# Kernel optimization log

Hardware: AMD Instinct MI355X
Metric: run time of the kernel (lower is better)

The kernel has to match this reference:

```python
import jax, jax.numpy as jnp
import numpy as np

B, LP, LQ, D, H = 4, 256, 256, 256, 256


def setup_inputs() -> dict:
    key = jax.random.key(0)
    ks = jax.random.split(key, 10)
    s_d = 1.0 / np.sqrt(D)
    s_h = 1.0 / np.sqrt(H)
    return {
        "Hp": jax.random.normal(ks[0], (B, LP, D), jnp.float32),
        "Hq": jax.random.normal(ks[1], (B, LQ, D), jnp.float32),
        # weights stored as (in, out); torch Linear does x @ W.T
        "Wc1": jax.random.normal(ks[2], (D, H), jnp.float32) * s_d,
        "Wc2": jax.random.normal(ks[3], (D, H), jnp.float32) * s_d,
        "vc": jax.random.normal(ks[4], (H,), jnp.float32) * s_h,
        "Wb": jax.random.normal(ks[5], (D, D), jnp.float32) * s_d,
        "Wd": jax.random.normal(ks[6], (D, H), jnp.float32) * s_d,
        "vd": jax.random.normal(ks[7], (H,), jnp.float32) * s_h,
        "Wm": jax.random.normal(ks[8], (D, H), jnp.float32) * s_d,
        "vm": jax.random.normal(ks[9], (H,), jnp.float32) * s_h,
    }


def _attend(scores, Hq):
    # scores: (B, Lp, Lq); softmax over Lq then weighted sum of Hq
    a = jax.nn.softmax(scores, axis=2)
    return jnp.einsum("bpq,bqd->bpd", a, Hq)


def reference(Hp, Hq, Wc1, Wc2, vc, Wb, Wd, vd, Wm, vm):
    # branch c: additive attention. tanh(Wc1 Hq + Wc2 Hp) . vc
    s1 = Hq @ Wc1                      # (B, Lq, H)
    s2 = Hp @ Wc2                      # (B, Lp, H)
    sc = jnp.einsum("bpqh,h->bpq", jnp.tanh(s1[:, None, :, :] + s2[:, :, None, :]), vc)
    qc = _attend(sc, Hq)

    # branch b: bilinear attention Hp (Wb Hq)^T
    sb = jnp.einsum("bpd,bqd->bpq", Hp, Hq @ Wb)
    qb = _attend(sb, Hq)

    # branch d: multiplicative interaction. tanh(Wd (Hq * Hp)) . vd
    sd = jnp.einsum("bpqh,h->bpq",
                    jnp.tanh(jnp.einsum("bqk,bpk,kh->bpqh", Hq, Hp, Wd)), vd)
    qd = _attend(sd, Hq)

    # branch m: subtractive interaction. tanh(Wm (Hq - Hp)) . vm
    m1 = Hq @ Wm                       # (B, Lq, H)
    m2 = Hp @ Wm                       # (B, Lp, H)
    sm = jnp.einsum("bpqh,h->bpq", jnp.tanh(m1[:, None, :, :] - m2[:, :, None, :]), vm)
    qm = _attend(sm, Hq)

    return (qc, qb, qd, qm)
```

## Files before the change

### kernel.cpp

```cpp
#include <hip/hip_runtime.h>

#define LOG2E 1.4426950408889634f
#define TANH_S 2.8853900817779268f
#define NB 4
#define NL 256
#define ND 256
#define NH 256

typedef __attribute__((ext_vector_type(8))) short s16x8;
typedef __attribute__((ext_vector_type(4))) short s16x4;
typedef __attribute__((ext_vector_type(4))) float f32x4;
typedef __attribute__((ext_vector_type(2))) unsigned int u32x2;
typedef __attribute__((ext_vector_type(4))) unsigned int u32x4;

static __device__ __forceinline__ float b2f(unsigned short u) {
  return __builtin_bit_cast(float, (unsigned int)u << 16);
}
static __device__ __forceinline__ unsigned short f2b(float f) {
  unsigned int x = __builtin_bit_cast(unsigned int, f);
  return (unsigned short)((x + 0x7fffu + ((x >> 16) & 1u)) >> 16);
}
static __device__ __forceinline__ unsigned int cvtpk(float lo, float hi) {
  unsigned int r;
  asm("v_cvt_pk_bf16_f32 %0, %1, %2" : "=v"(r) : "v"(lo), "v"(hi));
  return r;
}


__global__ void __launch_bounds__(256) prep(
    const float* __restrict__ Hq,
    const float* __restrict__ Wc1, const float* __restrict__ Wc2,
    const float* __restrict__ Wb, const float* __restrict__ Wm,
    const float* __restrict__ Wd, float* __restrict__ ws)
{
  const int which = blockIdx.y;
  const int tid = threadIdx.x;
  __shared__ __align__(16) float a_s[8][256];
  if (which == 0) {
    const int m0 = blockIdx.x * 8;
    unsigned short* AF = (unsigned short*)((char*)ws + 3145728);
    const int row = m0 + (tid >> 5);
    const int grp = tid & 31;
    const int kt = grp >> 2, quad = grp & 3;
    const int k0 = kt * 32 + quad * 8;
    const int bb = row >> 8, q = row & 255;
    const int w = q >> 6, mt = (q >> 4) & 3, c16 = q & 15;
    const float* src = Hq + row * ND + k0;
    f32x4 v0 = *(const f32x4*)(src);
    f32x4 v1 = *(const f32x4*)(src + 4);
    s16x8 o;
    #pragma unroll
    for (int j = 0; j < 4; ++j) { o[j] = (short)f2b(v0[j]); o[4 + j] = (short)f2b(v1[j]); }
    *(s16x8*)(AF + ((((bb * 4 + w) * 4 + mt) * 8 + kt) * 64 + quad * 16 + c16) * 8) = o;
    return;
  }
  if (which == 1) {
    if (blockIdx.x >= 32) return;
    const int k0 = blockIdx.x * 8;
    #pragma unroll
    for (int kk = 0; kk < 8; ++kk)
      a_s[kk][tid] = Wd[(k0 + kk) * NH + tid] * TANH_S;
    __syncthreads();
    float* WdT = (float*)((char*)ws + 4718592);
    f32x4 v0 = {a_s[0][tid], a_s[1][tid], a_s[2][tid], a_s[3][tid]};
    f32x4 v1 = {a_s[4][tid], a_s[5][tid], a_s[6][tid], a_s[7][tid]};
    *(f32x4*)(WdT + tid * 256 + k0) = v0;
    *(f32x4*)(WdT + tid * 256 + k0 + 4) = v1;
    return;
  }
  const int w = blockIdx.x >> 5;
  const int k0 = (blockIdx.x & 31) * 8;
  const float* W = (w == 0) ? Wc1 : (w == 1) ? Wm : (w == 2) ? Wb : Wc2;
  const float scale = (w == 2) ? 1.0f : TANH_S;
  #pragma unroll
  for (int kk = 0; kk < 8; ++kk)
    a_s[kk][tid] = W[(k0 + kk) * NH + tid] * scale;
  __syncthreads();
  unsigned short* WT = (unsigned short*)((char*)ws + 3670016) + w * 131072;
  s16x8 hi, lo;
  #pragma unroll
  for (int kk = 0; kk < 8; ++kk) {
    float v = a_s[kk][tid];
    unsigned short h = f2b(v);
    hi[kk] = (short)h;
    lo[kk] = (short)f2b(v - b2f(h));
  }
  *(s16x8*)(WT + tid * 256 + k0) = hi;
  *(s16x8*)(WT + 65536 + tid * 256 + k0) = lo;
}

__global__ void __launch_bounds__(256) gemm5(
    const float* __restrict__ Hq, const float* __restrict__ Hp,
    float* __restrict__ ws)
{
  const int rt = blockIdx.x, ct = blockIdx.y, mz = blockIdx.z;
  const int tid = threadIdx.x;
  const int wave = tid >> 6, lane = tid & 63;
  const int quad = lane >> 4, c16 = lane & 15;

  __shared__ __align__(16) char bs[32768];
  char* BsH = bs;
  char* BsL = bs + 16384;

  const int w = (mz == 4) ? 1 : ((mz == 3) ? 3 : mz);
  const float* A = (mz >= 3) ? Hp : Hq;
  const int n0 = ct * 32;

  {
    const unsigned short* WTw = (const unsigned short*)((const char*)ws + 3670016)
                                + w * 131072 + n0 * 256;
    const int soff = (tid & 31) * 16;
    #pragma unroll
    for (int i = 0; i < 4; ++i) {
      const int h = i * 8 + (tid >> 5);
      const int doff = h * 512 + (soff ^ ((h & 7) * 16));
      u32x4 vh = *(const u32x4*)((const char*)WTw + h * 512 + soff);
      u32x4 vl = *(const u32x4*)((const char*)WTw + 131072 + h * 512 + soff);
      *(u32x4*)(BsH + doff) = vh;
      *(u32x4*)(BsL + doff) = vl;
    }
  }

  const int row = rt * 64 + wave * 16 + c16;
  s16x8 ah[8], al[8];
  #pragma unroll
  for (int kt = 0; kt < 8; ++kt) {
    const float* src = A + row * ND + kt * 32 + quad * 8;
    f32x4 v0 = *(const f32x4*)(src);
    f32x4 v1 = *(const f32x4*)(src + 4);
    #pragma unroll
    for (int j = 0; j < 4; ++j) {
      unsigned short h0 = f2b(v0[j]);
      ah[kt][j] = (short)h0;
      al[kt][j] = (short)f2b(v0[j] - b2f(h0));
      unsigned short h1 = f2b(v1[j]);
      ah[kt][4 + j] = (short)h1;
      al[kt][4 + j] = (short)f2b(v1[j] - b2f(h1));
    }
  }
  __syncthreads();

  f32x4 acc[2];
  #pragma unroll
  for (int nt = 0; nt < 2; ++nt) acc[nt] = f32x4{0.f, 0.f, 0.f, 0.f};

  const int xswz = (c16 & 7) * 16;
  #pragma unroll
  for (int kt = 0; kt < 8; ++kt) {
    #pragma unroll
    for (int nt = 0; nt < 2; ++nt) {
      const int baddr = (nt * 16 + c16) * 512 + ((kt * 64 + quad * 16) ^ xswz);
      s16x8 bh = *(const s16x8*)(BsH + baddr);
      s16x8 bl = *(const s16x8*)(BsL + baddr);
      acc[nt] = __builtin_amdgcn_mfma_f32_16x16x32_bf16(ah[kt], bh, acc[nt], 0, 0, 0);
      acc[nt] = __builtin_amdgcn_mfma_f32_16x16x32_bf16(al[kt], bh, acc[nt], 0, 0, 0);
      acc[nt] = __builtin_amdgcn_mfma_f32_16x16x32_bf16(ah[kt], bl, acc[nt], 0, 0, 0);
    }
  }

  const int orow0 = rt * 64 + wave * 16 + quad * 4;
  if (mz == 2) {
    #pragma unroll
    for (int nt = 0; nt < 2; ++nt)
      #pragma unroll
      for (int r = 0; r < 4; ++r)
        ws[(orow0 + r) * NH + n0 + nt * 16 + c16] = acc[nt][r];
  } else {
    unsigned short* O = (unsigned short*)((char*)ws +
        (mz == 0 ? 1048576 : (mz == 1 ? 1572864 : (mz == 3 ? 2097152 : 2621440))));
    #pragma unroll
    for (int nt = 0; nt < 2; ++nt)
      #pragma unroll
      for (int r = 0; r < 4; ++r)
        O[(orow0 + r) * NH + n0 + nt * 16 + c16] = f2b(acc[nt][r]);
  }
}

__global__ void __launch_bounds__(256) dfused(
    const float* __restrict__ Hp, const float* __restrict__ Hq,
    const float* __restrict__ vd, const float* __restrict__ vc,
    const float* __restrict__ vm, const float* __restrict__ ws,
    float* __restrict__ out)
{
  const int p = blockIdx.x, b = blockIdx.y;
  const int tid = threadIdx.x;
  const int wave = tid >> 6, lane = tid & 63;
  const int quad = lane >> 4, c16 = lane & 15;

  __shared__ __align__(16) char ovl[33792];
  __shared__ __align__(16) float sc4[4 * 256];
  __shared__ __align__(16) float hp_s[256];
  __shared__ __align__(16) float invsum[4];

  short* Bs = (short*)ovl;
  float* vd2_s = (float*)(ovl + 32768);
  float* redp = (float*)ovl;
  float* c2_s = (float*)(ovl + 16384);
  float* m2_s = (float*)(ovl + 17408);
  float* vc2_s = (float*)(ovl + 18432);
  float* vm2_s = (float*)(ovl + 19456);

  const unsigned short* AF = (const unsigned short*)((const char*)ws + 3145728);
  const float* WdT = (const float*)((const char*)ws + 4718592);
  const float* X = ws;
  const unsigned short* C1  = (const unsigned short*)((const char*)ws + 1048576);
  const unsigned short* M1  = (const unsigned short*)((const char*)ws + 1572864);
  const unsigned short* C2b = (const unsigned short*)((const char*)ws + 2097152);
  const unsigned short* M2b = (const unsigned short*)((const char*)ws + 2621440);

  hp_s[tid] = Hp[(b * NL + p) * ND + tid];
  vd2_s[tid] = 2.0f * vd[tid];
  __syncthreads();

  {
    const int scol = (tid & 63) * 4;
    const f32x4 hpv = *(const f32x4*)(hp_s + scol);
    const int wq0 = wave * 64;
    const unsigned short* AFw = AF + (b * 4 + wave) * 4 * 8 * 64 * 8;
    const int xswz = (c16 & 7) * 16;

    float sdp[4][4];
    #pragma unroll
    for (int mt = 0; mt < 4; ++mt)
      #pragma unroll
      for (int r = 0; r < 4; ++r) sdp[mt][r] = 0.f;
    float vs2 = 0.f;

    for (int ht = 0; ht < 4; ++ht) {
      const int h0 = ht * 64;
      __syncthreads();
      {
        const float* wsrc = WdT + h0 * 256 + tid * 4;
        #pragma unroll
        for (int i = 0; i < 16; ++i) {
          f32x4 wv = *(const f32x4*)(wsrc + i * 1024);
          const int h = i * 4 + (tid >> 6);
          const unsigned int u0 = cvtpk(wv[0] * hpv[0], wv[1] * hpv[1]);
          const unsigned int u1 = cvtpk(wv[2] * hpv[2], wv[3] * hpv[3]);
          const int baddr = h * 512 + (((tid & 63) * 8) ^ ((h & 7) * 16));
          *(u32x2*)((char*)Bs + baddr) = u32x2{u0, u1};
        }
      }
      __syncthreads();

      f32x4 acc[4][4];
      #pragma unroll
      for (int mt = 0; mt < 4; ++mt)
        #pragma unroll
        for (int nt = 0; nt < 4; ++nt) acc[mt][nt] = f32x4{0.f, 0.f, 0.f, 0.f};

      #pragma unroll 2
      for (int kt = 0; kt < 8; ++kt) {
        s16x8 a8[4];
        #pragma unroll
        for (int mt = 0; mt < 4; ++mt)
          a8[mt] = *(const s16x8*)(AFw + ((mt * 8 + kt) * 64 + lane) * 8);
        #pragma unroll
        for (int nt = 0; nt < 4; ++nt) {
          const int baddr = (nt * 16 + c16) * 512 + ((kt * 64 + quad * 16) ^ xswz);
          s16x8 b8 = *(const s16x8*)((const char*)Bs + baddr);
          #pragma unroll
          for (int mt = 0; mt < 4; ++mt)
            acc[mt][nt] = __builtin_amdgcn_mfma_f32_16x16x32_bf16(
                a8[mt], b8, acc[mt][nt], 0, 0, 0);
        }
      }

      #pragma unroll
      for (int nt = 0; nt < 4; ++nt) {
        const float v2 = vd2_s[h0 + nt * 16 + c16];
        vs2 += v2;
        #pragma unroll
        for (int mt = 0; mt < 4; ++mt) {
          #pragma unroll
          for (int r = 0; r < 4; ++r) {
            float e = __builtin_amdgcn_exp2f(acc[mt][nt][r]);
            sdp[mt][r] += v2 * __builtin_amdgcn_rcpf(e + 1.0f);
          }
        }
      }
    }

    #pragma unroll
    for (int m = 1; m < 16; m <<= 1) vs2 += __shfl_xor(vs2, m, 64);
    #pragma unroll
    for (int mt = 0; mt < 4; ++mt)
      #pragma unroll
      for (int r = 0; r < 4; ++r) {
        float v = sdp[mt][r];
        #pragma unroll
        for (int m = 1; m < 16; m <<= 1) v += __shfl_xor(v, m, 64);
        if (c16 == 0)
          sc4[512 + wq0 + mt * 16 + quad * 4 + r] = 0.5f * vs2 - v;
      }
  }
  __syncthreads();

  {
    const int r = (b * NL + p) * ND + tid;
    c2_s[tid] = b2f(C2b[r]);
    m2_s[tid] = b2f(M2b[r]);
    vc2_s[tid] = 2.0f * vc[tid];
    vm2_s[tid] = 2.0f * vm[tid];
  }
  __syncthreads();

  {
    const int qsub = lane >> 4;
    const int hb = c16 * 4;
    float lc = 0.f, lm = 0.f;
    #pragma unroll
    for (int hi = 0; hi < 4; ++hi) {
      const int h = hb + hi * 64;
      #pragma unroll
      for (int i = 0; i < 4; ++i) { lc += vc2_s[h + i]; lm += vm2_s[h + i]; }
    }
    #pragma unroll
    for (int m = 1; m < 16; m <<= 1) {
      lc += __shfl_xor(lc, m, 64);
      lm += __shfl_xor(lm, m, 64);
    }
    const float c0 = 0.5f * lc, m0 = 0.5f * lm;

    for (int qg = 0; qg < 16; ++qg) {
      const int q = wave * 64 + qg * 4 + qsub;
      const unsigned short* c1r = C1 + (b * NL + q) * NH;
      const unsigned short* m1r = M1 + (b * NL + q) * NH;
      const float* xr = X + (b * NL + q) * ND;
      float pcr0 = 0.f, pmr0 = 0.f, pb0 = 0.f;
      float pcr1 = 0.f, pmr1 = 0.f, pb1 = 0.f;
      #pragma unroll
      for (int hi = 0; hi < 4; ++hi) {
        const int h = hb + hi * 64;
        s16x4 c1v = *(const s16x4*)(c1r + h);
        s16x4 m1v = *(const s16x4*)(m1r + h);
        f32x4 xv  = *(const f32x4*)(xr + h);
        #pragma unroll
        for (int i = 0; i < 4; ++i) {
          float ec = __builtin_amdgcn_exp2f(b2f((unsigned short)c1v[i]) + c2_s[h + i]);
          float em = __builtin_amdgcn_exp2f(b2f((unsigned short)m1v[i]) - m2_s[h + i]);
          if (i & 1) {
            pcr1 += vc2_s[h + i] * __builtin_amdgcn_rcpf(ec + 1.0f);
            pmr1 += vm2_s[h + i] * __builtin_amdgcn_rcpf(em + 1.0f);
            pb1 += hp_s[h + i] * xv[i];
          } else {
            pcr0 += vc2_s[h + i] * __builtin_amdgcn_rcpf(ec + 1.0f);
            pmr0 += vm2_s[h + i] * __builtin_amdgcn_rcpf(em + 1.0f);
            pb0 += hp_s[h + i] * xv[i];
          }
        }
      }
      float pcr = pcr0 + pcr1, pmr = pmr0 + pmr1, pb = pb0 + pb1;
      #pragma unroll
      for (int m = 1; m < 16; m <<= 1) {
        pcr += __shfl_xor(pcr, m, 64);
        pmr += __shfl_xor(pmr, m, 64);
        pb  += __shfl_xor(pb, m, 64);
      }
      if (c16 == 0) {
        sc4[q]       = c0 - pcr;
        sc4[256 + q] = pb;
        sc4[768 + q] = m0 - pmr;
      }
    }
  }
  __syncthreads();

  {
    float s0 = sc4[wave * 256 + lane];
    float s1 = sc4[wave * 256 + lane + 64];
    float s2 = sc4[wave * 256 + lane + 128];
    float s3 = sc4[wave * 256 + lane + 192];
    float mx = fmaxf(fmaxf(s0, s1), fmaxf(s2, s3));
    #pragma unroll
    for (int m = 1; m < 64; m <<= 1) mx = fmaxf(mx, __shfl_xor(mx, m, 64));
    float e0 = __builtin_amdgcn_exp2f((s0 - mx) * LOG2E);
    float e1 = __builtin_amdgcn_exp2f((s1 - mx) * LOG2E);
    float e2 = __builtin_amdgcn_exp2f((s2 - mx) * LOG2E);
    float e3 = __builtin_amdgcn_exp2f((s3 - mx) * LOG2E);
    float sm = e0 + e1 + e2 + e3;
    #pragma unroll
    for (int m = 1; m < 64; m <<= 1) sm += __shfl_xor(sm, m, 64);
    sc4[wave * 256 + lane]       = e0;
    sc4[wave * 256 + lane + 64]  = e1;
    sc4[wave * 256 + lane + 128] = e2;
    sc4[wave * 256 + lane + 192] = e3;
    if (lane == 0) invsum[wave] = __builtin_amdgcn_rcpf(sm);
  }
  __syncthreads();

  {
    const int q0 = wave * 64;
    f32x4 pa0 = {0.f,0.f,0.f,0.f}, pa1 = {0.f,0.f,0.f,0.f};
    f32x4 pa2 = {0.f,0.f,0.f,0.f}, pa3 = {0.f,0.f,0.f,0.f};
    for (int qi = 0; qi < 64; ++qi) {
      const int q = q0 + qi;
      const float ac = sc4[q];
      const float ab = sc4[256 + q];
      const float ad = sc4[512 + q];
      const float am = sc4[768 + q];
      f32x4 hv = *(const f32x4*)(Hq + (b * NL + q) * ND + lane * 4);
      pa0 += ac * hv; pa1 += ab * hv; pa2 += ad * hv; pa3 += am * hv;
    }
    *(f32x4*)(redp + (wave * 4 + 0) * 256 + lane * 4) = pa0;
    *(f32x4*)(redp + (wave * 4 + 1) * 256 + lane * 4) = pa1;
    *(f32x4*)(redp + (wave * 4 + 2) * 256 + lane * 4) = pa2;
    *(f32x4*)(redp + (wave * 4 + 3) * 256 + lane * 4) = pa3;
  }
  __syncthreads();

  {
    #pragma unroll
    for (int br = 0; br < 4; ++br) {
      float s = redp[(0 * 4 + br) * 256 + tid] + redp[(1 * 4 + br) * 256 + tid]
              + redp[(2 * 4 + br) * 256 + tid] + redp[(3 * 4 + br) * 256 + tid];
      out[((br * NB + b) * NL + p) * ND + tid] = s * invsum[br];
    }
  }
}

extern "C" void kernel_launch(void* const* d_in, const int* in_sizes, int n_in,
                              void* d_out, int out_size, void* d_ws, size_t ws_size,
                              hipStream_t stream) {
  const float* Hp  = (const float*)d_in[0];
  const float* Hq  = (const float*)d_in[1];
  const float* Wc1 = (const float*)d_in[2];
  const float* Wc2 = (const float*)d_in[3];
  const float* vc  = (const float*)d_in[4];
  const float* Wb  = (const float*)d_in[5];
  const float* Wd  = (const float*)d_in[6];
  const float* vd  = (const float*)d_in[7];
  const float* Wm  = (const float*)d_in[8];
  const float* vm  = (const float*)d_in[9];
  float* ws = (float*)d_ws;
  float* out = (float*)d_out;

  hipLaunchKernelGGL(prep, dim3(128, 3), dim3(256), 0, stream,
                     Hq, Wc1, Wc2, Wb, Wm, Wd, ws);
  hipLaunchKernelGGL(gemm5, dim3(16, 8, 5), dim3(256), 0, stream,
                     Hq, Hp, ws);
  hipLaunchKernelGGL(dfused, dim3(256, 4), dim3(256), 0, stream,
                     Hp, Hq, vd, vc, vm, ws, out);
}
```

Measured before the change: 190.0 us.

## Factor exp2 of additive/subtractive scores into precomputed per-row exponentials

Uses exp2(a+b)=exp2(a)*exp2(b). The q-side exponentials for the c and m branches are computed once in the GEMM epilogue and stored as fp32, and the p-side exponentials are computed once per block. This replaces a per-element transcendental in the inner loop with a multiply. The per-thread constants (vc2, vm2, hp, and the exp factors) are also hoisted into registers. The trade is double the bytes read for the C1/M1 operands and a risk of overflow or precision loss, since the exponentials are computed separately instead of on the summed argument.

```diff
diff --git a/kernel.cpp b/kernel.cpp
--- a/kernel.cpp
+++ b/kernel.cpp
@@ -61,7 +61,7 @@
     for (int kk = 0; kk < 8; ++kk)
       a_s[kk][tid] = Wd[(k0 + kk) * NH + tid] * TANH_S;
     __syncthreads();
-    float* WdT = (float*)((char*)ws + 4718592);
+    float* WdT = (float*)((char*)ws + 5767168);
     f32x4 v0 = {a_s[0][tid], a_s[1][tid], a_s[2][tid], a_s[3][tid]};
     f32x4 v1 = {a_s[4][tid], a_s[5][tid], a_s[6][tid], a_s[7][tid]};
     *(f32x4*)(WdT + tid * 256 + k0) = v0;
@@ -76,7 +76,7 @@
   for (int kk = 0; kk < 8; ++kk)
     a_s[kk][tid] = W[(k0 + kk) * NH + tid] * scale;
   __syncthreads();
-  unsigned short* WT = (unsigned short*)((char*)ws + 3670016) + w * 131072;
+  unsigned short* WT = (unsigned short*)((char*)ws + 4718592) + w * 131072;
   s16x8 hi, lo;
   #pragma unroll
   for (int kk = 0; kk < 8; ++kk) {
@@ -107,7 +107,7 @@
   const int n0 = ct * 32;
 
   {
-    const unsigned short* WTw = (const unsigned short*)((const char*)ws + 3670016)
+    const unsigned short* WTw = (const unsigned short*)((const char*)ws + 4718592)
                                 + w * 131072 + n0 * 256;
     const int soff = (tid & 31) * 16;
     #pragma unroll
@@ -165,9 +165,17 @@
       #pragma unroll
       for (int r = 0; r < 4; ++r)
         ws[(orow0 + r) * NH + n0 + nt * 16 + c16] = acc[nt][r];
+  } else if (mz < 2) {
+    float* E = (float*)((char*)ws + (mz == 0 ? 1048576 : 2097152));
+    #pragma unroll
+    for (int nt = 0; nt < 2; ++nt)
+      #pragma unroll
+      for (int r = 0; r < 4; ++r)
+        E[(orow0 + r) * NH + n0 + nt * 16 + c16] =
+            __builtin_amdgcn_exp2f(acc[nt][r]);
   } else {
     unsigned short* O = (unsigned short*)((char*)ws +
-        (mz == 0 ? 1048576 : (mz == 1 ? 1572864 : (mz == 3 ? 2097152 : 2621440))));
+        (mz == 3 ? 3670016 : 4194304));
     #pragma unroll
     for (int nt = 0; nt < 2; ++nt)
       #pragma unroll
@@ -195,18 +203,18 @@
   short* Bs = (short*)ovl;
   float* vd2_s = (float*)(ovl + 32768);
   float* redp = (float*)ovl;
-  float* c2_s = (float*)(ovl + 16384);
-  float* m2_s = (float*)(ovl + 17408);
+  float* e2c_s = (float*)(ovl + 16384);
+  float* e2m_s = (float*)(ovl + 17408);
   float* vc2_s = (float*)(ovl + 18432);
   float* vm2_s = (float*)(ovl + 19456);
 
   const unsigned short* AF = (const unsigned short*)((const char*)ws + 3145728);
-  const float* WdT = (const float*)((const char*)ws + 4718592);
+  const float* WdT = (const float*)((const char*)ws + 5767168);
   const float* X = ws;
-  const unsigned short* C1  = (const unsigned short*)((const char*)ws + 1048576);
-  const unsigned short* M1  = (const unsigned short*)((const char*)ws + 1572864);
-  const unsigned short* C2b = (const unsigned short*)((const char*)ws + 2097152);
-  const unsigned short* M2b = (const unsigned short*)((const char*)ws + 2621440);
+  const float* EC1 = (const float*)((const char*)ws + 1048576);
+  const float* EM1 = (const float*)((const char*)ws + 2097152);
+  const unsigned short* C2b = (const unsigned short*)((const char*)ws + 3670016);
+  const unsigned short* M2b = (const unsigned short*)((const char*)ws + 4194304);
 
   hp_s[tid] = Hp[(b * NL + p) * ND + tid];
   vd2_s[tid] = 2.0f * vd[tid];
@@ -298,8 +306,8 @@
 
   {
     const int r = (b * NL + p) * ND + tid;
-    c2_s[tid] = b2f(C2b[r]);
-    m2_s[tid] = b2f(M2b[r]);
+    e2c_s[tid] = __builtin_amdgcn_exp2f(b2f(C2b[r]));
+    e2m_s[tid] = __builtin_amdgcn_exp2f(-b2f(M2b[r]));
     vc2_s[tid] = 2.0f * vc[tid];
     vm2_s[tid] = 2.0f * vm[tid];
   }
@@ -308,12 +316,18 @@
   {
     const int qsub = lane >> 4;
     const int hb = c16 * 4;
+    f32x4 vc2v[4], vm2v[4], e2cv[4], e2mv[4], hpv4[4];
     float lc = 0.f, lm = 0.f;
     #pragma unroll
     for (int hi = 0; hi < 4; ++hi) {
       const int h = hb + hi * 64;
-      #pragma unroll
-      for (int i = 0; i < 4; ++i) { lc += vc2_s[h + i]; lm += vm2_s[h + i]; }
+      vc2v[hi] = *(const f32x4*)(vc2_s + h);
+      vm2v[hi] = *(const f32x4*)(vm2_s + h);
+      e2cv[hi] = *(const f32x4*)(e2c_s + h);
+      e2mv[hi] = *(const f32x4*)(e2m_s + h);
+      hpv4[hi] = *(const f32x4*)(hp_s + h);
+      #pragma unroll
+      for (int i = 0; i < 4; ++i) { lc += vc2v[hi][i]; lm += vm2v[hi][i]; }
     }
     #pragma unroll
     for (int m = 1; m < 16; m <<= 1) {
@@ -324,29 +338,29 @@
 
     for (int qg = 0; qg < 16; ++qg) {
       const int q = wave * 64 + qg * 4 + qsub;
-      const unsigned short* c1r = C1 + (b * NL + q) * NH;
-      const unsigned short* m1r = M1 + (b * NL + q) * NH;
-      const float* xr = X + (b * NL + q) * ND;
+      const float* ecr = EC1 + (b * NL + q) * NH;
+      const float* emr = EM1 + (b * NL + q) * NH;
+      const float* xr  = X + (b * NL + q) * ND;
       float pcr0 = 0.f, pmr0 = 0.f, pb0 = 0.f;
       float pcr1 = 0.f, pmr1 = 0.f, pb1 = 0.f;
       #pragma unroll
       for (int hi = 0; hi < 4; ++hi) {
         const int h = hb + hi * 64;
-        s16x4 c1v = *(const s16x4*)(c1r + h);
-        s16x4 m1v = *(const s16x4*)(m1r + h);
-        f32x4 xv  = *(const f32x4*)(xr + h);
+        f32x4 ec = *(const f32x4*)(ecr + h);
+        f32x4 em = *(const f32x4*)(emr + h);
+        f32x4 xv = *(const f32x4*)(xr + h);
         #pragma unroll
         for (int i = 0; i < 4; ++i) {
-          float ec = __builtin_amdgcn_exp2f(b2f((unsigned short)c1v[i]) + c2_s[h + i]);
-          float em = __builtin_amdgcn_exp2f(b2f((unsigned short)m1v[i]) - m2_s[h + i]);
+          float tc = ec[i] * e2cv[hi][i] + 1.0f;
+          float tm = em[i] * e2mv[hi][i] + 1.0f;
           if (i & 1) {
-            pcr1 += vc2_s[h + i] * __builtin_amdgcn_rcpf(ec + 1.0f);
-            pmr1 += vm2_s[h + i] * __builtin_amdgcn_rcpf(em + 1.0f);
-            pb1 += hp_s[h + i] * xv[i];
+            pcr1 += vc2v[hi][i] * __builtin_amdgcn_rcpf(tc);
+            pmr1 += vm2v[hi][i] * __builtin_amdgcn_rcpf(tm);
+            pb1 += hpv4[hi][i] * xv[i];
           } else {
-            pcr0 += vc2_s[h + i] * __builtin_amdgcn_rcpf(ec + 1.0f);
-            pmr0 += vm2_s[h + i] * __builtin_amdgcn_rcpf(em + 1.0f);
-            pb0 += hp_s[h + i] * xv[i];
+            pcr0 += vc2v[hi][i] * __builtin_amdgcn_rcpf(tc);
+            pmr0 += vm2v[hi][i] * __builtin_amdgcn_rcpf(tm);
+            pb0 += hpv4[hi][i] * xv[i];
           }
         }
       }
```

Measured after the change: 241.9 us. +27.3%, slower.
